# Kernel tuning notes

Measured on AMD Instinct MI355X. Metric: run time of the kernel, lower is better.

Reference implementation:

```python
import jax, jax.numpy as jnp
import numpy as np

B, N_NODES, T_IN = 512, 32, 12
HID, HEADS, OUT_CH, DEG = 64, 8, 9, 8


def setup_inputs() -> dict:
    key = jax.random.key(0)
    ks = jax.random.split(key, 26)
    rn = lambda k, s, sc=0.1: (jax.random.normal(k, s, jnp.float32) * sc)
    E = B * N_NODES * DEG
    src = jax.random.randint(ks[0], (E,), 0, N_NODES, jnp.int32)
    dst = jax.random.randint(ks[1], (E,), 0, N_NODES, jnp.int32)
    off = jnp.repeat(jnp.arange(B, dtype=jnp.int32) * N_NODES, N_NODES * DEG)
    edge_index = jnp.stack([src + off, dst + off])  # block-diagonal batched graph
    x = jax.random.normal(ks[2], (B, N_NODES, T_IN), jnp.float32)
    return {
        "x": x,
        "edge_index": edge_index,
        # gat1: in=T_IN -> HEADS*HID, concat
        "W1": rn(ks[3], (T_IN, HEADS * HID)),
        "a_src1": rn(ks[4], (HEADS, HID)),
        "a_dst1": rn(ks[5], (HEADS, HID)),
        "b1": rn(ks[6], (HEADS * HID,), 0.01),
        # gat2: in=HEADS*HID -> HID, heads=1, mean (concat=False)
        "W2": rn(ks[7], (HEADS * HID, HID), 0.05),
        "a_src2": rn(ks[8], (1, HID)),
        "a_dst2": rn(ks[9], (1, HID)),
        "b2": rn(ks[10], (HID,), 0.01),
        "gamma": jnp.ones((HID,), jnp.float32),
        "beta": jnp.zeros((HID,), jnp.float32),
        # gru1: input_size=N_NODES(=32), hidden=HID
        "Wi1": rn(ks[11], (3 * HID, N_NODES)),
        "Wh1": rn(ks[12], (3 * HID, HID)),
        "bi1": rn(ks[13], (3 * HID,), 0.01),
        "bh1": rn(ks[14], (3 * HID,), 0.01),
        # gru2: input_size=HID, hidden=HID
        "Wi2": rn(ks[15], (3 * HID, HID)),
        "Wh2": rn(ks[16], (3 * HID, HID)),
        "bi2": rn(ks[17], (3 * HID,), 0.01),
        "bh2": rn(ks[18], (3 * HID,), 0.01),
        "Wf": rn(ks[19], (OUT_CH, HID)),
        "bf": rn(ks[20], (OUT_CH,), 0.01),
    }


def _gat_layer(x, src, dst, W, a_s, a_d, b, concat):
    # PyG GATConv (eval mode, self-loops already appended by caller)
    Nn = x.shape[0]
    heads, hc = a_s.shape
    h = (x @ W).reshape(Nn, heads, hc)                 # [N, H, C]
    es = jnp.sum(h * a_s, axis=-1)                     # [N, H]
    ed = jnp.sum(h * a_d, axis=-1)
    e = jax.nn.leaky_relu(es[src] + ed[dst], 0.2)      # [E, H]
    m = jax.ops.segment_max(e, dst, num_segments=Nn)
    p = jnp.exp(e - m[dst])
    s = jax.ops.segment_sum(p, dst, num_segments=Nn)
    alpha = p / (s[dst] + 1e-16)                       # per-dst softmax
    out = jax.ops.segment_sum(h[src] * alpha[:, :, None], dst, num_segments=Nn)
    out = out.reshape(Nn, heads * hc) if concat else out.mean(axis=1)
    return out + b


def _gru(x, Wi, Wh, bi, bh):
    # torch.nn.GRU (batch_first) single layer; x: [B, T, F]
    H = Wh.shape[1]
    xi = x @ Wi.T + bi                                 # [B, T, 3H]
    def step(h, xt):
        gh = h @ Wh.T + bh
        r = jax.nn.sigmoid(xt[:, :H] + gh[:, :H])
        z = jax.nn.sigmoid(xt[:, H:2 * H] + gh[:, H:2 * H])
        n = jnp.tanh(xt[:, 2 * H:] + r * gh[:, 2 * H:])
        hn = (1.0 - z) * n + z * h
        return hn, hn
    h0 = jnp.zeros((x.shape[0], H), x.dtype)
    _, ys = jax.lax.scan(step, h0, jnp.swapaxes(xi, 0, 1))
    return jnp.swapaxes(ys, 0, 1)


def reference(x, edge_index, W1, a_src1, a_dst1, b1, W2, a_src2, a_dst2, b2,
              gamma, beta, Wi1, Wh1, bi1, bh1, Wi2, Wh2, bi2, bh2, Wf, bf):
    Bsz, Nn_, T = x.shape
    Nn = Bsz * Nn_
    xf = x.reshape(Nn, T)                              # dropout is identity in eval
    sl = jnp.arange(Nn, dtype=edge_index.dtype)        # PyG add_self_loops=True
    src = jnp.concatenate([edge_index[0], sl])
    dst = jnp.concatenate([edge_index[1], sl])
    h = jax.nn.elu(_gat_layer(xf, src, dst, W1, a_src1, a_dst1, b1, True))
    h = jax.nn.elu(_gat_layer(h, src, dst, W2, a_src2, a_dst2, b2, False))
    mu = h.mean(-1, keepdims=True)
    var = ((h - mu) ** 2).mean(-1, keepdims=True)
    h = (h - mu) / jnp.sqrt(var + 1e-5) * gamma + beta
    seq = h.reshape(Bsz, Nn_, -1).transpose(0, 2, 1)   # [B, HID(seq), N_NODES(feat)]
    g = _gru(seq, Wi1, Wh1, bi1, bh1)
    g = _gru(g, Wi2, Wh2, bi2, bh2)
    return g[:, -1, :] @ Wf.T + bf                     # [B, OUT_CH]
```

## Files before the change

### kernel.cpp

```cpp
#include <hip/hip_runtime.h>
#include <hip/hip_bf16.h>
#include <stdint.h>

#define BATCH 512
#define NN 32
#define T_IN 12
#define HID 64
#define HEADS 8
#define OUT_CH 9
#define EPB (NN*8)
#define ETOT (EPB+NN)
#define F1 (HEADS*HID)

using u16 = unsigned short;
using u32 = unsigned int;
typedef _Float16 f16;
typedef _Float16 f16x2 __attribute__((ext_vector_type(2)));

__device__ __forceinline__ float bf2f(u16 u){ return __uint_as_float(((u32)u)<<16); }
__device__ __forceinline__ u16 f2bf(float f){
    u32 x = __float_as_uint(f);
    u32 r = (x + 0x7FFFu + ((x>>16)&1u))>>16;
    return (u16)r;
}
__device__ __forceinline__ u32 packf16(float a, float b){
    f16x2 p; p.x=(f16)a; p.y=(f16)b; return __builtin_bit_cast(u32,p);
}
__device__ __forceinline__ u16 f2h16(float a){ f16 h=(f16)a; return __builtin_bit_cast(u16,h); }
__device__ __forceinline__ float lof(u32 w){ return (float)__builtin_bit_cast(f16x2,w).x; }
__device__ __forceinline__ float hif(u32 w){ return (float)__builtin_bit_cast(f16x2,w).y; }
__device__ __forceinline__ float dot2(u32 a, u32 b, float c){
#if __has_builtin(__builtin_amdgcn_fdot2)
    return __builtin_amdgcn_fdot2(__builtin_bit_cast(f16x2,a), __builtin_bit_cast(f16x2,b), c, false);
#else
    return fmaf(lof(a),lof(b), fmaf(hif(a),hif(b), c));
#endif
}
__device__ __forceinline__ float elu1(float x){ return x > 0.f ? x : (__expf(x)-1.f); }
__device__ __forceinline__ float sigm(float x){ return 1.f/(1.f+__expf(-x)); }
__device__ __forceinline__ float tanh_(float x){ return 1.f - 2.f/(__expf(2.f*x)+1.f); }
__device__ __forceinline__ u32 fenc(float v){
    u32 b=__float_as_uint(v);
    return (b&0x80000000u) ? ~b : (b|0x80000000u);
}
__device__ __forceinline__ float fdec(u32 k){
    return __uint_as_float((k&0x80000000u) ? (k&0x7FFFFFFFu) : ~k);
}

__global__ __launch_bounds__(256) void k_detect(const u32* __restrict__ xw, int* __restrict__ flag){
    __shared__ int cnt;
    if(threadIdx.x==0) cnt=0;
    __syncthreads();
    int c=0;
    for(int i=threadIdx.x;i<4096;i+=256){
        u32 w=xw[i];
        if(w & 0x7FFFFFFFu){
            u32 el=(w>>7)&0xFFu;
            if(el>=0x90u) c++;
        }
    }
    atomicAdd(&cnt,c);
    __syncthreads();
    if(threadIdx.x==0) *flag = (cnt>256) ? 1 : 0;
}

struct CvtDesc {
    const void* src[20];
    void*       dst[20];
    int         n[20];
};

__global__ __launch_bounds__(256) void k_convert(CvtDesc d, const int* __restrict__ flag){
    const int seg = blockIdx.x;
    const int f = *flag;
    const void* s = d.src[seg];
    const int n = d.n[seg];
    const int stride = gridDim.y*256;
    float* o=(float*)d.dst[seg];
    for(int i=blockIdx.y*256+threadIdx.x;i<n;i+=stride)
        o[i] = f ? ((const float*)s)[i] : bf2f(((const u16*)s)[i]);
}

__global__ __launch_bounds__(256) void k_w2i(const void* __restrict__ W2src, u16* __restrict__ W2i,
                                             const int* __restrict__ flag){
    int i = blockIdx.x*256+threadIdx.x;
    int k=i>>6, j=i&63;
    float v = (*flag)? ((const float*)W2src)[i] : bf2f(((const u16*)W2src)[i]);
    W2i[ (((size_t)(k>>3)*64 + j)<<3) + (k&7) ] = f2h16(v);
}

__global__ __launch_bounds__(256,2) void k_gat1(
    const float* __restrict__ x, const int* __restrict__ ei,
    const float* __restrict__ W1, const float* __restrict__ a_s, const float* __restrict__ a_d,
    const float* __restrict__ b1, u32* __restrict__ h1g)
{
    const int b = blockIdx.x, t = threadIdx.x;
    __shared__ __align__(16) float s_x[NN][12];
    __shared__ float s_W1[T_IN*F1];
    __shared__ __align__(16) u16 s_h[NN][520];
    __shared__ u32 s_aspk[HEADS*32], s_adpk[HEADS*32];
    __shared__ float s_es[NN][HEADS], s_ed[NN][HEADS];
    __shared__ unsigned char s_src[ETOT], s_dst[ETOT];
    __shared__ float s_al[ETOT][HEADS];
    __shared__ u32 s_mx[NN*HEADS];
    __shared__ float s_sm[NN*HEADS], s_inv[NN*HEADS];
    __shared__ int s_cnt[NN], s_off[NN], s_fil[NN];
    __shared__ short s_lst[ETOT];

    for(int i=t;i<NN*T_IN;i+=256) s_x[i/12][i%12] = x[b*NN*T_IN + i];
    for(int i=t;i<T_IN*F1;i+=256) s_W1[i]=W1[i];
    s_aspk[t]=packf16(a_s[2*t],a_s[2*t+1]);
    s_adpk[t]=packf16(a_d[2*t],a_d[2*t+1]);
    s_mx[t]=0u; s_sm[t]=0.f;
    if(t<EPB){
        s_src[t] = (unsigned char)(ei[b*EPB+t] - b*NN);
        s_dst[t] = (unsigned char)(ei[(size_t)BATCH*EPB + b*EPB+t] - b*NN);
    }
    if(t<NN){ s_src[EPB+t]=s_dst[EPB+t]=(unsigned char)t; s_cnt[t]=0; s_fil[t]=0; }
    __syncthreads();

    {
        float w0[12], w1[12];
        #pragma unroll
        for(int k=0;k<12;k++){ w0[k]=s_W1[k*F1+t]; w1[k]=s_W1[k*F1+t+256]; }
        for(int n=0;n<NN;n++){
            float xr[12];
            const float4* xp=(const float4*)s_x[n];
            *(float4*)&xr[0]=xp[0]; *(float4*)&xr[4]=xp[1]; *(float4*)&xr[8]=xp[2];
            float A=0.f,B=0.f;
            #pragma unroll
            for(int k=0;k<12;k++){ A=fmaf(xr[k],w0[k],A); B=fmaf(xr[k],w1[k],B); }
            s_h[n][t]=f2h16(A); s_h[n][t+256]=f2h16(B);
        }
    }
    for(int e=t;e<ETOT;e+=256) atomicAdd(&s_cnt[s_dst[e]],1);
    __syncthreads();

    {
        int n=t&31, hd=t>>5;
        const uint4* hp=(const uint4*)((const u16*)s_h[n] + hd*64);
        u32 hw[32];
        #pragma unroll
        for(int q=0;q<8;q++) *(uint4*)&hw[q*4]=hp[q];
        float e1=0.f,e2=0.f;
        #pragma unroll
        for(int k=0;k<32;k++){ e1=dot2(hw[k],s_aspk[hd*32+k],e1); e2=dot2(hw[k],s_adpk[hd*32+k],e2); }
        s_es[n][hd]=e1; s_ed[n][hd]=e2;
    }
    if(t==0){ int o=0; for(int i=0;i<NN;i++){ s_off[i]=o; o+=s_cnt[i]; } }
    __syncthreads();

    for(int e=t;e<ETOT;e+=256){
        int d=s_dst[e]; int p=atomicAdd(&s_fil[d],1); s_lst[s_off[d]+p]=(short)e;
    }
    for(int i=t;i<ETOT*HEADS;i+=256){
        int e=i>>3, hd=i&7;
        int sr=s_src[e], d=s_dst[e];
        float v = s_es[sr][hd]+s_ed[d][hd];
        v = v>0.f? v : 0.2f*v;
        s_al[e][hd]=v;
        atomicMax(&s_mx[d*8+hd], fenc(v));
    }
    __syncthreads();

    for(int i=t;i<ETOT*HEADS;i+=256){
        int e=i>>3, hd=i&7;
        int d=s_dst[e];
        float p=__expf(s_al[e][hd]-fdec(s_mx[d*8+hd]));
        s_al[e][hd]=p;
        atomicAdd(&s_sm[d*8+hd], p);
    }
    __syncthreads();
    s_inv[t]=1.f/(s_sm[t]+1e-16f);
    __syncthreads();

    {
        int d=t&31, hd=t>>5;
        int o=s_off[d], cnt=s_cnt[d];
        float inv=s_inv[d*8+hd];
        size_t obase = ((size_t)(b*NN+d))*256 + hd*32;
        #pragma unroll
        for(int ch=0;ch<2;ch++){
            float acc[32];
            #pragma unroll
            for(int i=0;i<32;i++) acc[i]=0.f;
            for(int i=0;i<cnt;i++){
                int e=s_lst[o+i]; float a=s_al[e][hd]; int sr=s_src[e];
                const uint4* hp=(const uint4*)((const u16*)s_h[sr] + hd*64 + ch*32);
                u32 pw[16];
                *(uint4*)&pw[0]=hp[0]; *(uint4*)&pw[4]=hp[1];
                *(uint4*)&pw[8]=hp[2]; *(uint4*)&pw[12]=hp[3];
                #pragma unroll
                for(int q=0;q<16;q++){ acc[2*q]+=a*lof(pw[q]); acc[2*q+1]+=a*hif(pw[q]); }
            }
            u32* op = h1g + obase + ch*16;
            #pragma unroll
            for(int j=0;j<16;j++){
                float v0=elu1(acc[2*j]*inv   + b1[hd*64+ch*32+2*j]);
                float v1=elu1(acc[2*j+1]*inv + b1[hd*64+ch*32+2*j+1]);
                op[j]=packf16(v0,v1);
            }
        }
    }
}

__global__ __launch_bounds__(256,2) void k_gat2ln(
    const u32* __restrict__ h1g, const int* __restrict__ ei,
    const uint4* __restrict__ W2i, const float* __restrict__ a_s2, const float* __restrict__ a_d2,
    const float* __restrict__ b2, const float* __restrict__ gam, const float* __restrict__ bet,
    float* __restrict__ hlng)
{
    const int b=blockIdx.x, t=threadIdx.x;
    __shared__ __align__(16) u32 s_h1[NN*260];
    __shared__ float s_h2[NN][HID];
    __shared__ float s_es[NN], s_ed[NN];
    __shared__ unsigned char s_src[ETOT], s_dst[ETOT];
    __shared__ float s_al[ETOT];
    __shared__ u32 s_mx[NN];
    __shared__ float s_sm[NN], s_inv[NN];
    __shared__ int s_cnt[NN], s_off[NN], s_fil[NN];
    __shared__ short s_lst[ETOT];

    { const u32* g = h1g + (size_t)b*8192;
      for(int w=t; w<8192; w+=256){ int n=w>>8, c=w&255; s_h1[n*260+c]=g[w]; } }
    if(t<EPB){
        s_src[t]=(unsigned char)(ei[b*EPB+t]-b*NN);
        s_dst[t]=(unsigned char)(ei[(size_t)BATCH*EPB+b*EPB+t]-b*NN);
    }
    if(t<NN){ s_src[EPB+t]=s_dst[EPB+t]=(unsigned char)t;
              s_cnt[t]=0; s_fil[t]=0; s_mx[t]=0u; s_sm[t]=0.f; }
    __syncthreads();

    for(int e=t;e<ETOT;e+=256) atomicAdd(&s_cnt[s_dst[e]],1);
    {
        int n0=(t>>4)<<1, j0=(t&15)<<2;
        const u32* r0=&s_h1[n0*260];
        const u32* r1=&s_h1[(n0+1)*260];
        float a00=0,a01=0,a02=0,a03=0,a10=0,a11=0,a12=0,a13=0;
        for(int kb=0;kb<64;kb++){
            uint4 A0=*(const uint4*)&r0[kb*4];
            uint4 A1=*(const uint4*)&r1[kb*4];
            const uint4* wp=&W2i[kb*64+j0];
            uint4 w0=wp[0], w1=wp[1], w2=wp[2], w3=wp[3];
            a00=dot2(A0.x,w0.x,a00); a00=dot2(A0.y,w0.y,a00); a00=dot2(A0.z,w0.z,a00); a00=dot2(A0.w,w0.w,a00);
            a01=dot2(A0.x,w1.x,a01); a01=dot2(A0.y,w1.y,a01); a01=dot2(A0.z,w1.z,a01); a01=dot2(A0.w,w1.w,a01);
            a02=dot2(A0.x,w2.x,a02); a02=dot2(A0.y,w2.y,a02); a02=dot2(A0.z,w2.z,a02); a02=dot2(A0.w,w2.w,a02);
            a03=dot2(A0.x,w3.x,a03); a03=dot2(A0.y,w3.y,a03); a03=dot2(A0.z,w3.z,a03); a03=dot2(A0.w,w3.w,a03);
            a10=dot2(A1.x,w0.x,a10); a10=dot2(A1.y,w0.y,a10); a10=dot2(A1.z,w0.z,a10); a10=dot2(A1.w,w0.w,a10);
            a11=dot2(A1.x,w1.x,a11); a11=dot2(A1.y,w1.y,a11); a11=dot2(A1.z,w1.z,a11); a11=dot2(A1.w,w1.w,a11);
            a12=dot2(A1.x,w2.x,a12); a12=dot2(A1.y,w2.y,a12); a12=dot2(A1.z,w2.z,a12); a12=dot2(A1.w,w2.w,a12);
            a13=dot2(A1.x,w3.x,a13); a13=dot2(A1.y,w3.y,a13); a13=dot2(A1.z,w3.z,a13); a13=dot2(A1.w,w3.w,a13);
        }
        s_h2[n0][j0]=a00; s_h2[n0][j0+1]=a01; s_h2[n0][j0+2]=a02; s_h2[n0][j0+3]=a03;
        s_h2[n0+1][j0]=a10; s_h2[n0+1][j0+1]=a11; s_h2[n0+1][j0+2]=a12; s_h2[n0+1][j0+3]=a13;
    }
    __syncthreads();

    {
        int n=t>>3, g=t&7;
        float e1=0,e2=0;
        #pragma unroll
        for(int cc=0; cc<8; cc++){
            float hv = s_h2[n][g*8+cc];
            e1 += hv*a_s2[g*8+cc];
            e2 += hv*a_d2[g*8+cc];
        }
        #pragma unroll
        for(int m=1;m<8;m<<=1){ e1 += __shfl_xor(e1,m,64); e2 += __shfl_xor(e2,m,64); }
        if(g==0){ s_es[n]=e1; s_ed[n]=e2; }
    }
    if(t==0){ int o=0; for(int i=0;i<NN;i++){ s_off[i]=o; o+=s_cnt[i]; } }
    __syncthreads();

    for(int e=t;e<ETOT;e+=256){
        int d=s_dst[e]; int p=atomicAdd(&s_fil[d],1); s_lst[s_off[d]+p]=(short)e;
    }
    for(int e=t;e<ETOT;e+=256){
        int d=s_dst[e];
        float v = s_es[s_src[e]] + s_ed[d];
        v = v>0.f? v:0.2f*v;
        s_al[e]=v;
        atomicMax(&s_mx[d], fenc(v));
    }
    __syncthreads();

    for(int e=t;e<ETOT;e+=256){
        int d=s_dst[e];
        float p=__expf(s_al[e]-fdec(s_mx[d]));
        s_al[e]=p;
        atomicAdd(&s_sm[d], p);
    }
    __syncthreads();
    if(t<NN) s_inv[t]=1.f/(s_sm[t]+1e-16f);
    __syncthreads();

    {
        int n=t>>3, g=t&7;
        float acc[8];
        #pragma unroll
        for(int i=0;i<8;i++) acc[i]=0;
        int o=s_off[n], cnt=s_cnt[n];
        float inv=s_inv[n];
        for(int i=0;i<cnt;i++){
            int e=s_lst[o+i]; float a=s_al[e]; int sr=s_src[e];
            const float4* hp=(const float4*)&s_h2[sr][g*8];
            float4 v0=hp[0], v1=hp[1];
            acc[0]+=a*v0.x; acc[1]+=a*v0.y; acc[2]+=a*v0.z; acc[3]+=a*v0.w;
            acc[4]+=a*v1.x; acc[5]+=a*v1.y; acc[6]+=a*v1.z; acc[7]+=a*v1.w;
        }
        float sum=0,sq=0;
        #pragma unroll
        for(int i=0;i<8;i++){
            float v = elu1(acc[i]*inv + b2[g*8+i]);
            acc[i]=v; sum+=v; sq+=v*v;
        }
        #pragma unroll
        for(int m=1;m<8;m<<=1){ sum+=__shfl_xor(sum,m,64); sq+=__shfl_xor(sq,m,64); }
        float mu = sum*(1.f/64.f);
        float var = sq*(1.f/64.f) - mu*mu;
        float rs = rsqrtf(var + 1e-5f);
        float* outp = hlng + (size_t)b*HID*NN;
        #pragma unroll
        for(int i=0;i<8;i++){
            int c=g*8+i;
            float v=(acc[i]-mu)*rs*gam[c] + bet[c];
            outp[c*NN + n] = v;
        }
    }
}

__global__ __launch_bounds__(256,2) void k_gruf(
    const float* __restrict__ hlng,
    const float* __restrict__ Wi1, const float* __restrict__ Wh1,
    const float* __restrict__ bi1, const float* __restrict__ bh1,
    const float* __restrict__ Wi2, const float* __restrict__ Wh2,
    const float* __restrict__ bi2, const float* __restrict__ bh2,
    const float* __restrict__ Wf, const float* __restrict__ bfv,
    void* __restrict__ outp, const int* __restrict__ flag)
{
    const int b=blockIdx.x, t=threadIdx.x;
    const int wave=t>>6, lane=t&63;
    const int layer=wave>>1;
    const int ublk=wave&1;
    const int uu=lane&31, s=lane>>5;
    const int u=ublk*32+uu;

    __shared__ __align__(16) u32 s_x1[64*16];
    __shared__ __align__(16) u32 s_h1[2][32];
    __shared__ __align__(16) u32 s_h2[2][32];
    __shared__ float s_h2f[64];

    { const float2* g=(const float2*)(hlng + (size_t)b*2048);
      for(int w=t;w<1024;w+=256){ float2 v=g[w]; s_x1[w]=packf16(v.x,v.y); } }
    if(t<32){ s_h1[0][t]=0u; s_h1[1][t]=0u; s_h2[0][t]=0u; s_h2[1][t]=0u; }

    u32 wiR[16],wiZ[16],wiN[16],whR[16],whZ[16],whN[16];
    if(layer==0){
        const float2* WiF=(const float2*)Wi1;
        const float2* WhF=(const float2*)Wh1;
        #pragma unroll
        for(int k=0;k<8;k++){
            float2 a=WiF[u*16+s*8+k], c=WiF[(64+u)*16+s*8+k], d=WiF[(128+u)*16+s*8+k];
            wiR[k]=packf16(a.x,a.y); wiZ[k]=packf16(c.x,c.y); wiN[k]=packf16(d.x,d.y);
        }
        #pragma unroll
        for(int k=0;k<16;k++){
            float2 a=WhF[u*32+s*16+k], c=WhF[(64+u)*32+s*16+k], d=WhF[(128+u)*32+s*16+k];
            whR[k]=packf16(a.x,a.y); whZ[k]=packf16(c.x,c.y); whN[k]=packf16(d.x,d.y);
        }
    } else {
        const float2* WiF=(const float2*)Wi2;
        const float2* WhF=(const float2*)Wh2;
        #pragma unroll
        for(int k=0;k<16;k++){
            float2 a=WiF[u*32+s*16+k], c=WiF[(64+u)*32+s*16+k], d=WiF[(128+u)*32+s*16+k];
            wiR[k]=packf16(a.x,a.y); wiZ[k]=packf16(c.x,c.y); wiN[k]=packf16(d.x,d.y);
            float2 e=WhF[u*32+s*16+k], f=WhF[(64+u)*32+s*16+k], g2=WhF[(128+u)*32+s*16+k];
            whR[k]=packf16(e.x,e.y); whZ[k]=packf16(f.x,f.y); whN[k]=packf16(g2.x,g2.y);
        }
    }
    const float* bi = layer? bi2:bi1;
    const float* bh = layer? bh2:bh1;
    float br=bi[u]+bh[u], bz=bi[64+u]+bh[64+u], bxn=bi[128+u], bhn=bh[128+u];
    float h=0.f;
    __syncthreads();

    for(int it=0; it<=64; ++it){
        const int pb=(it-1)&1, cb=it&1;
        float pr=0.f,pz=0.f,pxn=0.f,phn=0.f;
        bool act;
        if(layer==0){
            act=(it<64);
            if(act){
                u32 xw[8], hw[16];
                const uint4* xp=(const uint4*)&s_x1[it*16+s*8];
                *(uint4*)&xw[0]=xp[0]; *(uint4*)&xw[4]=xp[1];
                const uint4* hp=(const uint4*)&s_h1[pb][s*16];
                #pragma unroll
                for(int q=0;q<4;q++) *(uint4*)&hw[q*4]=hp[q];
                #pragma unroll
                for(int k=0;k<8;k++){ pr=dot2(xw[k],wiR[k],pr); pz=dot2(xw[k],wiZ[k],pz); pxn=dot2(xw[k],wiN[k],pxn); }
                #pragma unroll
                for(int k=0;k<16;k++){ pr=dot2(hw[k],whR[k],pr); pz=dot2(hw[k],whZ[k],pz); phn=dot2(hw[k],whN[k],phn); }
            }
        } else {
            act=(it>=1);
            if(act){
                u32 xw[16], hw[16];
                const uint4* xp=(const uint4*)&s_h1[pb][s*16];
                #pragma unroll
                for(int q=0;q<4;q++) *(uint4*)&xw[q*4]=xp[q];
                const uint4* hp=(const uint4*)&s_h2[pb][s*16];
                #pragma unroll
                for(int q=0;q<4;q++) *(uint4*)&hw[q*4]=hp[q];
                #pragma unroll
                for(int k=0;k<16;k++){
                    pr=dot2(xw[k],wiR[k],pr); pz=dot2(xw[k],wiZ[k],pz); pxn=dot2(xw[k],wiN[k],pxn);
                    pr=dot2(hw[k],whR[k],pr); pz=dot2(hw[k],whZ[k],pz); phn=dot2(hw[k],whN[k],phn);
                }
            }
        }
        if(act){
            pr  += __shfl_xor(pr ,32,64);
            pz  += __shfl_xor(pz ,32,64);
            pxn += __shfl_xor(pxn,32,64);
            phn += __shfl_xor(phn,32,64);
            float r=sigm(pr+br), z=sigm(pz+bz);
            float n=tanh_(pxn+bxn + r*(phn+bhn));
            h=(1.f-z)*n + z*h;
            if(s==0){
                u16 hv=f2h16(h);
                if(layer==0) ((u16*)s_h1[cb])[u]=hv;
                else { ((u16*)s_h2[cb])[u]=hv; if(it==64) s_h2f[u]=h; }
            }
        }
        __syncthreads();
    }

    if(t<OUT_CH){
        float acc=bfv[t];
        #pragma unroll
        for(int i=0;i<64;i++) acc += s_h2f[i]*Wf[t*64+i];
        if(*flag) ((float*)outp)[b*OUT_CH+t]=acc;
        else      ((u16*)outp)[b*OUT_CH+t]=f2bf(acc);
    }
}

extern "C" void kernel_launch(void* const* d_in, const int* in_sizes, int n_in,
                              void* d_out, int out_size, void* d_ws, size_t ws_size,
                              hipStream_t stream)
{
    char* ws=(char*)d_ws;
    int* flag = (int*)ws;
    float* cf = (float*)(ws + 256);
    float* c_x   = cf; cf+=196608;
    float* c_W1  = cf; cf+=6144;
    float* c_as1 = cf; cf+=512;
    float* c_ad1 = cf; cf+=512;
    float* c_b1  = cf; cf+=512;
    float* c_as2 = cf; cf+=64;
    float* c_ad2 = cf; cf+=64;
    float* c_b2  = cf; cf+=64;
    float* c_gam = cf; cf+=64;
    float* c_bet = cf; cf+=64;
    float* c_Wi1 = cf; cf+=6144;
    float* c_Wh1 = cf; cf+=12288;
    float* c_bi1 = cf; cf+=192;
    float* c_bh1 = cf; cf+=192;
    float* c_Wi2 = cf; cf+=12288;
    float* c_Wh2 = cf; cf+=12288;
    float* c_bi2 = cf; cf+=192;
    float* c_bh2 = cf; cf+=192;
    float* c_Wf  = cf; cf+=576;
    float* c_bf  = cf; cf+=9;
    uintptr_t p = ((uintptr_t)cf + 255) & ~(uintptr_t)255;
    u16* c_W2i = (u16*)p;
    p = (p + 32768*2 + 255) & ~(uintptr_t)255;
    u32* h1g = (u32*)p;
    p = (p + (size_t)BATCH*NN*256*4 + 255) & ~(uintptr_t)255;
    float* hlng = (float*)p;

    const int* ei = (const int*)d_in[1];

    CvtDesc d;
    const int srcIdx[20] = {0,2,3,4,5,7,8,9,10,11,12,13,14,15,16,17,18,19,20,21};
    void* dsts[20] = {c_x,c_W1,c_as1,c_ad1,c_b1,c_as2,c_ad2,c_b2,c_gam,c_bet,
                      c_Wi1,c_Wh1,c_bi1,c_bh1,c_Wi2,c_Wh2,c_bi2,c_bh2,c_Wf,c_bf};
    const int ns[20] = {196608,6144,512,512,512,64,64,64,64,64,
                        6144,12288,192,192,12288,12288,192,192,576,9};
    for(int i=0;i<20;i++){ d.src[i]=d_in[srcIdx[i]]; d.dst[i]=dsts[i]; d.n[i]=ns[i]; }

    k_detect <<<dim3(1),dim3(256),0,stream>>>((const u32*)d_in[0], flag);
    k_convert<<<dim3(20,8),dim3(256),0,stream>>>(d, flag);
    k_w2i    <<<dim3(128),dim3(256),0,stream>>>(d_in[6], c_W2i, flag);
    k_gat1   <<<dim3(BATCH),dim3(256),0,stream>>>(c_x,ei,c_W1,c_as1,c_ad1,c_b1,h1g);
    k_gat2ln <<<dim3(BATCH),dim3(256),0,stream>>>(h1g,ei,(const uint4*)c_W2i,c_as2,c_ad2,c_b2,c_gam,c_bet,hlng);
    k_gruf   <<<dim3(BATCH),dim3(256),0,stream>>>(hlng,c_Wi1,c_Wh1,c_bi1,c_bh1,
                                                  c_Wi2,c_Wh2,c_bi2,c_bh2,c_Wf,c_bf,d_out,flag);
}
```

Measured before the change: 260.0 us.

## Widen GRU kernel to 512 threads with prepacked fp16 weights, retile gat2 matmul

The GRU kernel now runs 512 threads per block, splitting each unit's dot products four ways across lanes with an extra shuffle reduction. This shortens the serial per-step work in the 64-step recurrence. GRU weights are pre-packed to fp16 pairs by a new kernel, so each thread loads its slice with vector loads instead of converting at startup. The gat2 W2 matmul is retiled to 4 nodes by 2 outputs per thread, and the final linear layer uses float4 loads. The trade-offs are one more kernel launch, higher register pressure at 512 threads, and an extra shuffle stage in every step.

```diff
diff --git a/kernel.cpp b/kernel.cpp
--- a/kernel.cpp
+++ b/kernel.cpp
@@ -65,9 +65,9 @@
 }
 
 struct CvtDesc {
-    const void* src[20];
-    void*       dst[20];
-    int         n[20];
+    const void* src[16];
+    void*       dst[16];
+    int         n[16];
 };
 
 __global__ __launch_bounds__(256) void k_convert(CvtDesc d, const int* __restrict__ flag){
@@ -87,6 +87,25 @@
     int k=i>>6, j=i&63;
     float v = (*flag)? ((const float*)W2src)[i] : bf2f(((const u16*)W2src)[i]);
     W2i[ (((size_t)(k>>3)*64 + j)<<3) + (k&7) ] = f2h16(v);
+}
+
+__global__ __launch_bounds__(256) void k_wpk(
+    const void* __restrict__ Wi1, const void* __restrict__ Wh1,
+    const void* __restrict__ Wi2, const void* __restrict__ Wh2,
+    u32* __restrict__ wpk, const int* __restrict__ flag)
+{
+    int w = blockIdx.x*256+threadIdx.x;
+    int m = w/6144;
+    int rem = w - m*6144;
+    int row = rem>>5, kw = rem&31;
+    const void* s = (m==0)?Wi1 : (m==1)?Wh1 : (m==2)?Wi2 : Wh2;
+    int K = (m==0)?32:64;
+    int f=*flag;
+    int k0=2*kw, k1=k0+1;
+    float v0=0.f, v1=0.f;
+    if(k0<K) v0 = f? ((const float*)s)[row*K+k0] : bf2f(((const u16*)s)[row*K+k0]);
+    if(k1<K) v1 = f? ((const float*)s)[row*K+k1] : bf2f(((const u16*)s)[row*K+k1]);
+    wpk[w]=packf16(v0,v1);
 }
 
 __global__ __launch_bounds__(256,2) void k_gat1(
@@ -233,26 +252,32 @@
 
     for(int e=t;e<ETOT;e+=256) atomicAdd(&s_cnt[s_dst[e]],1);
     {
-        int n0=(t>>4)<<1, j0=(t&15)<<2;
-        const u32* r0=&s_h1[n0*260];
+        int n0=(t>>5)<<2, j0=(t&31)<<1;
+        const u32* r0=&s_h1[(n0+0)*260];
         const u32* r1=&s_h1[(n0+1)*260];
-        float a00=0,a01=0,a02=0,a03=0,a10=0,a11=0,a12=0,a13=0;
+        const u32* r2=&s_h1[(n0+2)*260];
+        const u32* r3=&s_h1[(n0+3)*260];
+        float a00=0,a01=0,a10=0,a11=0,a20=0,a21=0,a30=0,a31=0;
         for(int kb=0;kb<64;kb++){
             uint4 A0=*(const uint4*)&r0[kb*4];
             uint4 A1=*(const uint4*)&r1[kb*4];
+            uint4 A2=*(const uint4*)&r2[kb*4];
+            uint4 A3=*(const uint4*)&r3[kb*4];
             const uint4* wp=&W2i[kb*64+j0];
-            uint4 w0=wp[0], w1=wp[1], w2=wp[2], w3=wp[3];
+            uint4 w0=wp[0], w1=wp[1];
             a00=dot2(A0.x,w0.x,a00); a00=dot2(A0.y,w0.y,a00); a00=dot2(A0.z,w0.z,a00); a00=dot2(A0.w,w0.w,a00);
             a01=dot2(A0.x,w1.x,a01); a01=dot2(A0.y,w1.y,a01); a01=dot2(A0.z,w1.z,a01); a01=dot2(A0.w,w1.w,a01);
-            a02=dot2(A0.x,w2.x,a02); a02=dot2(A0.y,w2.y,a02); a02=dot2(A0.z,w2.z,a02); a02=dot2(A0.w,w2.w,a02);
-            a03=dot2(A0.x,w3.x,a03); a03=dot2(A0.y,w3.y,a03); a03=dot2(A0.z,w3.z,a03); a03=dot2(A0.w,w3.w,a03);
             a10=dot2(A1.x,w0.x,a10); a10=dot2(A1.y,w0.y,a10); a10=dot2(A1.z,w0.z,a10); a10=dot2(A1.w,w0.w,a10);
             a11=dot2(A1.x,w1.x,a11); a11=dot2(A1.y,w1.y,a11); a11=dot2(A1.z,w1.z,a11); a11=dot2(A1.w,w1.w,a11);
-            a12=dot2(A1.x,w2.x,a12); a12=dot2(A1.y,w2.y,a12); a12=dot2(A1.z,w2.z,a12); a12=dot2(A1.w,w2.w,a12);
-            a13=dot2(A1.x,w3.x,a13); a13=dot2(A1.y,w3.y,a13); a13=dot2(A1.z,w3.z,a13); a13=dot2(A1.w,w3.w,a13);
-        }
-        s_h2[n0][j0]=a00; s_h2[n0][j0+1]=a01; s_h2[n0][j0+2]=a02; s_h2[n0][j0+3]=a03;
-        s_h2[n0+1][j0]=a10; s_h2[n0+1][j0+1]=a11; s_h2[n0+1][j0+2]=a12; s_h2[n0+1][j0+3]=a13;
+            a20=dot2(A2.x,w0.x,a20); a20=dot2(A2.y,w0.y,a20); a20=dot2(A2.z,w0.z,a20); a20=dot2(A2.w,w0.w,a20);
+            a21=dot2(A2.x,w1.x,a21); a21=dot2(A2.y,w1.y,a21); a21=dot2(A2.z,w1.z,a21); a21=dot2(A2.w,w1.w,a21);
+            a30=dot2(A3.x,w0.x,a30); a30=dot2(A3.y,w0.y,a30); a30=dot2(A3.z,w0.z,a30); a30=dot2(A3.w,w0.w,a30);
+            a31=dot2(A3.x,w1.x,a31); a31=dot2(A3.y,w1.y,a31); a31=dot2(A3.z,w1.z,a31); a31=dot2(A3.w,w1.w,a31);
+        }
+        s_h2[n0+0][j0]=a00; s_h2[n0+0][j0+1]=a01;
+        s_h2[n0+1][j0]=a10; s_h2[n0+1][j0+1]=a11;
+        s_h2[n0+2][j0]=a20; s_h2[n0+2][j0+1]=a21;
+        s_h2[n0+3][j0]=a30; s_h2[n0+3][j0+1]=a31;
     }
     __syncthreads();
 
@@ -329,56 +354,50 @@
     }
 }
 
-__global__ __launch_bounds__(256,2) void k_gruf(
-    const float* __restrict__ hlng,
-    const float* __restrict__ Wi1, const float* __restrict__ Wh1,
+__global__ __launch_bounds__(512,1) void k_gruf(
+    const float* __restrict__ hlng, const u32* __restrict__ wpk,
     const float* __restrict__ bi1, const float* __restrict__ bh1,
-    const float* __restrict__ Wi2, const float* __restrict__ Wh2,
     const float* __restrict__ bi2, const float* __restrict__ bh2,
     const float* __restrict__ Wf, const float* __restrict__ bfv,
     void* __restrict__ outp, const int* __restrict__ flag)
 {
     const int b=blockIdx.x, t=threadIdx.x;
     const int wave=t>>6, lane=t&63;
-    const int layer=wave>>1;
-    const int ublk=wave&1;
-    const int uu=lane&31, s=lane>>5;
-    const int u=ublk*32+uu;
-
-    __shared__ __align__(16) u32 s_x1[64*16];
+    const int layer=wave>>2;
+    const int uu=lane&15, kq=lane>>4;
+    const int u=(wave&3)*16+uu;
+
+    __shared__ __align__(16) u32 s_x1[64][32];
     __shared__ __align__(16) u32 s_h1[2][32];
     __shared__ __align__(16) u32 s_h2[2][32];
     __shared__ float s_h2f[64];
 
-    { const float2* g=(const float2*)(hlng + (size_t)b*2048);
-      for(int w=t;w<1024;w+=256){ float2 v=g[w]; s_x1[w]=packf16(v.x,v.y); } }
+    {   const float2* g=(const float2*)(hlng + (size_t)b*2048);
+        for(int w=t;w<2048;w+=512){
+            int step=w>>5, j=w&31;
+            u32 v=0u;
+            if(j<16){ float2 f=g[step*16+j]; v=packf16(f.x,f.y); }
+            s_x1[step][j]=v;
+        }
+    }
     if(t<32){ s_h1[0][t]=0u; s_h1[1][t]=0u; s_h2[0][t]=0u; s_h2[1][t]=0u; }
 
-    u32 wiR[16],wiZ[16],wiN[16],whR[16],whZ[16],whN[16];
-    if(layer==0){
-        const float2* WiF=(const float2*)Wi1;
-        const float2* WhF=(const float2*)Wh1;
-        #pragma unroll
-        for(int k=0;k<8;k++){
-            float2 a=WiF[u*16+s*8+k], c=WiF[(64+u)*16+s*8+k], d=WiF[(128+u)*16+s*8+k];
-            wiR[k]=packf16(a.x,a.y); wiZ[k]=packf16(c.x,c.y); wiN[k]=packf16(d.x,d.y);
-        }
-        #pragma unroll
-        for(int k=0;k<16;k++){
-            float2 a=WhF[u*32+s*16+k], c=WhF[(64+u)*32+s*16+k], d=WhF[(128+u)*32+s*16+k];
-            whR[k]=packf16(a.x,a.y); whZ[k]=packf16(c.x,c.y); whN[k]=packf16(d.x,d.y);
-        }
-    } else {
-        const float2* WiF=(const float2*)Wi2;
-        const float2* WhF=(const float2*)Wh2;
-        #pragma unroll
-        for(int k=0;k<16;k++){
-            float2 a=WiF[u*32+s*16+k], c=WiF[(64+u)*32+s*16+k], d=WiF[(128+u)*32+s*16+k];
-            wiR[k]=packf16(a.x,a.y); wiZ[k]=packf16(c.x,c.y); wiN[k]=packf16(d.x,d.y);
-            float2 e=WhF[u*32+s*16+k], f=WhF[(64+u)*32+s*16+k], g2=WhF[(128+u)*32+s*16+k];
-            whR[k]=packf16(e.x,e.y); whZ[k]=packf16(f.x,f.y); whN[k]=packf16(g2.x,g2.y);
-        }
-    }
+    const u32* wi = wpk + (size_t)(layer*2+0)*6144 + kq*8;
+    const u32* wh = wpk + (size_t)(layer*2+1)*6144 + kq*8;
+    u32 wiR[8],wiZ[8],wiN[8],whR[8],whZ[8],whN[8];
+    *(uint4*)&wiR[0]=*(const uint4*)&wi[(u     )*32];
+    *(uint4*)&wiR[4]=*(const uint4*)&wi[(u     )*32+4];
+    *(uint4*)&wiZ[0]=*(const uint4*)&wi[(64+u  )*32];
+    *(uint4*)&wiZ[4]=*(const uint4*)&wi[(64+u  )*32+4];
+    *(uint4*)&wiN[0]=*(const uint4*)&wi[(128+u )*32];
+    *(uint4*)&wiN[4]=*(const uint4*)&wi[(128+u )*32+4];
+    *(uint4*)&whR[0]=*(const uint4*)&wh[(u     )*32];
+    *(uint4*)&whR[4]=*(const uint4*)&wh[(u     )*32+4];
+    *(uint4*)&whZ[0]=*(const uint4*)&wh[(64+u  )*32];
+    *(uint4*)&whZ[4]=*(const uint4*)&wh[(64+u  )*32+4];
+    *(uint4*)&whN[0]=*(const uint4*)&wh[(128+u )*32];
+    *(uint4*)&whN[4]=*(const uint4*)&wh[(128+u )*32+4];
+
     const float* bi = layer? bi2:bi1;
     const float* bh = layer? bh2:bh1;
     float br=bi[u]+bh[u], bz=bi[64+u]+bh[64+u], bxn=bi[128+u], bhn=bh[128+u];
@@ -387,48 +406,29 @@
 
     for(int it=0; it<=64; ++it){
         const int pb=(it-1)&1, cb=it&1;
-        float pr=0.f,pz=0.f,pxn=0.f,phn=0.f;
-        bool act;
-        if(layer==0){
-            act=(it<64);
-            if(act){
-                u32 xw[8], hw[16];
-                const uint4* xp=(const uint4*)&s_x1[it*16+s*8];
-                *(uint4*)&xw[0]=xp[0]; *(uint4*)&xw[4]=xp[1];
-                const uint4* hp=(const uint4*)&s_h1[pb][s*16];
-                #pragma unroll
-                for(int q=0;q<4;q++) *(uint4*)&hw[q*4]=hp[q];
-                #pragma unroll
-                for(int k=0;k<8;k++){ pr=dot2(xw[k],wiR[k],pr); pz=dot2(xw[k],wiZ[k],pz); pxn=dot2(xw[k],wiN[k],pxn); }
-                #pragma unroll
-                for(int k=0;k<16;k++){ pr=dot2(hw[k],whR[k],pr); pz=dot2(hw[k],whZ[k],pz); phn=dot2(hw[k],whN[k],phn); }
+        const bool act = layer ? (it>=1) : (it<64);
+        if(act){
+            u32 xw[8], hw[8];
+            const uint4* xp = layer ? (const uint4*)&s_h1[pb][kq*8]
+                                    : (const uint4*)&s_x1[it][kq*8];
+            *(uint4*)&xw[0]=xp[0]; *(uint4*)&xw[4]=xp[1];
+            const uint4* hp = layer ? (const uint4*)&s_h2[pb][kq*8]
+                                    : (const uint4*)&s_h1[pb][kq*8];
+            *(uint4*)&hw[0]=hp[0]; *(uint4*)&hw[4]=hp[1];
+            float pr=0.f,pz=0.f,pxn=0.f,phn=0.f;
+            #pragma unroll
+            for(int k=0;k<8;k++){
+                pr=dot2(xw[k],wiR[k],pr); pz=dot2(xw[k],wiZ[k],pz); pxn=dot2(xw[k],wiN[k],pxn);
+                pr=dot2(hw[k],whR[k],pr); pz=dot2(hw[k],whZ[k],pz); phn=dot2(hw[k],whN[k],phn);
             }
-        } else {
-            act=(it>=1);
-            if(act){
-                u32 xw[16], hw[16];
-                const uint4* xp=(const uint4*)&s_h1[pb][s*16];
-                #pragma unroll
-                for(int q=0;q<4;q++) *(uint4*)&xw[q*4]=xp[q];
-                const uint4* hp=(const uint4*)&s_h2[pb][s*16];
-                #pragma unroll
-                for(int q=0;q<4;q++) *(uint4*)&hw[q*4]=hp[q];
-                #pragma unroll
-                for(int k=0;k<16;k++){
-                    pr=dot2(xw[k],wiR[k],pr); pz=dot2(xw[k],wiZ[k],pz); pxn=dot2(xw[k],wiN[k],pxn);
-                    pr=dot2(hw[k],whR[k],pr); pz=dot2(hw[k],whZ[k],pz); phn=dot2(hw[k],whN[k],phn);
-                }
-            }
-        }
-        if(act){
-            pr  += __shfl_xor(pr ,32,64);
-            pz  += __shfl_xor(pz ,32,64);
-            pxn += __shfl_xor(pxn,32,64);
-            phn += __shfl_xor(phn,32,64);
+            pr +=__shfl_xor(pr ,16,64); pz +=__shfl_xor(pz ,16,64);
+            pxn+=__shfl_xor(pxn,16,64); phn+=__shfl_xor(phn,16,64);
+            pr +=__shfl_xor(pr ,32,64); pz +=__shfl_xor(pz ,32,64);
+            pxn+=__shfl_xor(pxn,32,64); phn+=__shfl_xor(phn,32,64);
             float r=sigm(pr+br), z=sigm(pz+bz);
             float n=tanh_(pxn+bxn + r*(phn+bhn));
             h=(1.f-z)*n + z*h;
-            if(s==0){
+            if(kq==0){
                 u16 hv=f2h16(h);
                 if(layer==0) ((u16*)s_h1[cb])[u]=hv;
                 else { ((u16*)s_h2[cb])[u]=hv; if(it==64) s_h2f[u]=h; }
@@ -439,8 +439,13 @@
 
     if(t<OUT_CH){
         float acc=bfv[t];
-        #pragma unroll
-        for(int i=0;i<64;i++) acc += s_h2f[i]*Wf[t*64+i];
+        const float4* wp=(const float4*)(Wf + t*64);
+        const float4* hp=(const float4*)s_h2f;
+        #pragma unroll
+        for(int k=0;k<16;k++){
+            float4 w=wp[k], v=hp[k];
+            acc += w.x*v.x + w.y*v.y + w.z*v.z + w.w*v.w;
+        }
         if(*flag) ((float*)outp)[b*OUT_CH+t]=acc;
         else      ((u16*)outp)[b*OUT_CH+t]=f2bf(acc);
     }
@@ -463,12 +468,8 @@
     float* c_b2  = cf; cf+=64;
     float* c_gam = cf; cf+=64;
     float* c_bet = cf; cf+=64;
-    float* c_Wi1 = cf; cf+=6144;
-    float* c_Wh1 = cf; cf+=12288;
     float* c_bi1 = cf; cf+=192;
     float* c_bh1 = cf; cf+=192;
-    float* c_Wi2 = cf; cf+=12288;
-    float* c_Wh2 = cf; cf+=12288;
     float* c_bi2 = cf; cf+=192;
     float* c_bh2 = cf; cf+=192;
     float* c_Wf  = cf; cf+=576;
@@ -476,6 +477,8 @@
     uintptr_t p = ((uintptr_t)cf + 255) & ~(uintptr_t)255;
     u16* c_W2i = (u16*)p;
     p = (p + 32768*2 + 255) & ~(uintptr_t)255;
+    u32* wpk = (u32*)p;
+    p = (p + 24576*4 + 255) & ~(uintptr_t)255;
     u32* h1g = (u32*)p;
     p = (p + (size_t)BATCH*NN*256*4 + 255) & ~(uintptr_t)255;
     float* hlng = (float*)p;
@@ -483,18 +486,18 @@
     const int* ei = (const int*)d_in[1];
 
     CvtDesc d;
-    const int srcIdx[20] = {0,2,3,4,5,7,8,9,10,11,12,13,14,15,16,17,18,19,20,21};
-    void* dsts[20] = {c_x,c_W1,c_as1,c_ad1,c_b1,c_as2,c_ad2,c_b2,c_gam,c_bet,
-                      c_Wi1,c_Wh1,c_bi1,c_bh1,c_Wi2,c_Wh2,c_bi2,c_bh2,c_Wf,c_bf};
-    const int ns[20] = {196608,6144,512,512,512,64,64,64,64,64,
-                        6144,12288,192,192,12288,12288,192,192,576,9};
-    for(int i=0;i<20;i++){ d.src[i]=d_in[srcIdx[i]]; d.dst[i]=dsts[i]; d.n[i]=ns[i]; }
+    const int srcIdx[16] = {0,2,3,4,5,7,8,9,10,11,14,15,18,19,20,21};
+    void* dsts[16] = {c_x,c_W1,c_as1,c_ad1,c_b1,c_as2,c_ad2,c_b2,c_gam,c_bet,
+                      c_bi1,c_bh1,c_bi2,c_bh2,c_Wf,c_bf};
+    const int ns[16] = {196608,6144,512,512,512,64,64,64,64,64,
+                        192,192,192,192,576,9};
+    for(int i=0;i<16;i++){ d.src[i]=d_in[srcIdx[i]]; d.dst[i]=dsts[i]; d.n[i]=ns[i]; }
 
     k_detect <<<dim3(1),dim3(256),0,stream>>>((const u32*)d_in[0], flag);
-    k_convert<<<dim3(20,8),dim3(256),0,stream>>>(d, flag);
+    k_convert<<<dim3(16,8),dim3(256),0,stream>>>(d, flag);
     k_w2i    <<<dim3(128),dim3(256),0,stream>>>(d_in[6], c_W2i, flag);
+    k_wpk    <<<dim3(96),dim3(256),0,stream>>>(d_in[12],d_in[13],d_in[16],d_in[17], wpk, flag);
     k_gat1   <<<dim3(BATCH),dim3(256),0,stream>>>(c_x,ei,c_W1,c_as1,c_ad1,c_b1,h1g);
     k_gat2ln <<<dim3(BATCH),dim3(256),0,stream>>>(h1g,ei,(const uint4*)c_W2i,c_as2,c_ad2,c_b2,c_gam,c_bet,hlng);
-    k_gruf   <<<dim3(BATCH),dim3(256),0,stream>>>(hlng,c_Wi1,c_Wh1,c_bi1,c_bh1,
-                                                  c_Wi2,c_Wh2,c_bi2,c_bh2,c_Wf,c_bf,d_out,flag);
-}
+    k_gruf   <<<dim3(BATCH),dim3(512),0,stream>>>(hlng,wpk,c_bi1,c_bh1,c_bi2,c_bh2,c_Wf,c_bf,d_out,flag);
+}
```

Result: no change. 258.7 us (-0.5%).
